# Kernel tuning notes

Measured on AMD Instinct MI355X. Metric: run time of the kernel, lower is better.

The kernel has to match this reference:

```python
import jax, jax.numpy as jnp
import numpy as np

K = 499  # kernel_size


def setup_inputs() -> dict:
    key = jax.random.key(0)
    k1, k2 = jax.random.split(key)
    B, F, T = 32, 64, 8000
    # nonnegative spectrogram input, shape (B, 1, F, T)
    x = jax.random.uniform(k1, (B, 1, F, T), dtype=jnp.float32)
    a = 0.90 + 0.099 * jax.random.uniform(k2, (F,), dtype=jnp.float32)
    w = jnp.ones((F,), dtype=jnp.float32)
    return {"x": x, "a": a, "w": w}


def _build_kernel(a, w, dtype):
    # powers[f, k] = a_f ** k, k = 0..K-2
    F = a.shape[0]
    powers = a[:, None] ** jnp.arange(K - 1, dtype=dtype)  # (F, K-1)
    C = 1.0 / powers.sum(axis=1)                            # (F,)
    neg = (-C * w)[:, None] * powers                        # (F, K-1)
    # pre-flip kernel = [1, neg_0, ..., neg_{K-2}]; flipped -> [neg_{K-2}, ..., neg_0, 1]
    kern = jnp.concatenate([neg[:, ::-1], jnp.ones((F, 1), dtype)], axis=1)  # (F, K)
    return kern[:, None, :]  # (F, 1, K) OIH, groups = F


def reference(x, a, w):
    dtype = x.dtype
    kern = _build_kernel(a.astype(dtype), w.astype(dtype), dtype)
    xs = x[:, 0]  # (B, F, T)
    # replicate (edge) pad on the left by K-1 along time
    xp = jnp.pad(xs, ((0, 0), (0, 0), (K - 1, 0)), mode="edge")
    y = jax.lax.conv_general_dilated(
        xp, kern,
        window_strides=(1,), padding="VALID",
        dimension_numbers=("NCH", "OIH", "NCH"),
        feature_group_count=xs.shape[1],
    )  # (B, F, T)
    return jnp.abs(y)[:, None]  # (B, 1, F, T)
```

## Files before the change

kernel.cpp:

```cpp
#include <hip/hip_runtime.h>
#include <math.h>


constexpr int T    = 8000;
constexpr int F    = 64;
constexpr int B    = 32;
constexpr int KM1  = 498;
constexpr int ROUND = 256;
constexpr int NROUND = (T + ROUND - 1) / ROUND;

__global__ __launch_bounds__(256) void willmore_scan_kernel(
    const float* __restrict__ x, const float* __restrict__ a,
    const float* __restrict__ w, float* __restrict__ out)
{
    const int wid  = (blockIdx.x * blockDim.x + threadIdx.x) >> 6;
    const int lane = threadIdx.x & 63;
    if (wid >= B * F) return;
    const int f = wid % F;

    const float* xr   = x   + (size_t)wid * T;
    float*       orow = out + (size_t)wid * T;

    const double ad = (double)a[f];
    double p = ad, a498d = 1.0;
    for (int e = KM1; e; e >>= 1) { if (e & 1) a498d *= p; p *= p; }
    const double sumgeo = (1.0 - a498d) / (1.0 - ad);
    const float  af     = (float)ad;
    const float  na498  = (float)(-a498d);
    const float  g      = (float)(1.0 / sumgeo) * w[f];
    const double a4d    = ad * ad * ad * ad;
    const float  alane  = (float)exp2(log2(a4d) * (double)lane);
    float wstep[6];
    double tpow = a4d;
    #pragma unroll
    for (int s = 0; s < 6; ++s) { wstep[s] = (float)tpow; tpow *= tpow; }
    const float a256 = (float)tpow;

    float S = xr[0] * (float)sumgeo;

    int tR = 0;
    for (int rnd = 0; rnd < NROUND; ++rnd, tR += ROUND) {
        const int tbase = tR + 4 * lane;
        const bool tail = (tR + ROUND > T);

        float4 xv;
        if (!tail) {
            xv = *(const float4*)(xr + tbase);
        } else {
            xv.x = xr[min(tbase,     T - 1)];
            xv.y = xr[min(tbase + 1, T - 1)];
            xv.z = xr[min(tbase + 2, T - 1)];
            xv.w = xr[min(tbase + 3, T - 1)];
        }

        const int lag = tbase - KM1;
        float l0, l1, l2, l3;
        if (lag >= 0 && !tail) {
            const float2* lp = (const float2*)(xr + lag);
            float2 la = lp[0], lb = lp[1];
            l0 = la.x; l1 = la.y; l2 = lb.x; l3 = lb.y;
        } else {
            l0 = xr[max(min(lag,     T - 1), 0)];
            l1 = xr[max(min(lag + 1, T - 1), 0)];
            l2 = xr[max(min(lag + 2, T - 1), 0)];
            l3 = xr[max(min(lag + 3, T - 1), 0)];
        }

        const float u0 = fmaf(na498, l0, xv.x);
        const float u1 = fmaf(na498, l1, xv.y);
        const float u2 = fmaf(na498, l2, xv.z);
        const float u3 = fmaf(na498, l3, xv.w);

        const float q0 = u0;
        const float q1 = fmaf(af, q0, u1);
        const float q2 = fmaf(af, q1, u2);
        const float q3 = fmaf(af, q2, u3);

        float G = q3;
        #pragma unroll
        for (int s = 0; s < 6; ++s) {
            const float gup = __shfl_up(G, 1 << s, 64);
            const float ws  = (lane >= (1 << s)) ? wstep[s] : 0.0f;
            G = fmaf(ws, gup, G);
        }
        float Gprev = __shfl_up(G, 1, 64);
        if (lane == 0) Gprev = 0.0f;

        float s0 = fmaf(alane, S, Gprev);
        const float y0 = fabsf(fmaf(-g, s0, xv.x));
        const float s1 = fmaf(af, s0, u0);
        const float y1 = fabsf(fmaf(-g, s1, xv.y));
        const float s2 = fmaf(af, s1, u1);
        const float y2 = fabsf(fmaf(-g, s2, xv.z));
        const float s3 = fmaf(af, s2, u2);
        const float y3 = fabsf(fmaf(-g, s3, xv.w));

        const float Slast = __shfl(G, 63, 64);
        S = fmaf(a256, S, Slast);

        if (!tail || (tbase + 3 < T)) {
            *(float4*)(orow + tbase) = make_float4(y0, y1, y2, y3);
        }
    }
}

extern "C" void kernel_launch(void* const* d_in, const int* in_sizes, int n_in,
                              void* d_out, int out_size, void* d_ws, size_t ws_size,
                              hipStream_t stream) {
    const float* x = (const float*)d_in[0];
    const float* a = (const float*)d_in[1];
    const float* w = (const float*)d_in[2];
    float* out = (float*)d_out;

    const int rows = B * F;
    const int threads = 256;
    const int blocks = rows * 64 / threads;
    hipLaunchKernelGGL(willmore_scan_kernel, dim3(blocks), dim3(threads), 0, stream,
                       x, a, w, out);
}
```

Before: 132.8 us.

## Split each row's scan into four time segments with windowed state initialization

Each row is now handled by one 256-thread block whose four wavefronts each scan a quarter of the time axis, instead of one wavefront scanning the whole row. Because the filter has finite support of 498 taps, each segment rebuilds its starting state directly from the preceding 512 samples using a weighted wavefront reduction. This shortens the serial chain of rounds per wavefront by about four times and should expose more latency hiding. The cost is some extra loads and arithmetic for the warm-up window, and possible precision differences from computing the initial state in float.

```diff
diff --git a/kernel.cpp b/kernel.cpp
--- a/kernel.cpp
+++ b/kernel.cpp
@@ -2,24 +2,27 @@
 #include <math.h>
 
 
-constexpr int T    = 8000;
-constexpr int F    = 64;
-constexpr int B    = 32;
-constexpr int KM1  = 498;
+constexpr int T     = 8000;
+constexpr int F     = 64;
+constexpr int B     = 32;
+constexpr int KM1   = 498;
+constexpr int NSEG  = 4;
+constexpr int SEGLEN = T / NSEG;
 constexpr int ROUND = 256;
-constexpr int NROUND = (T + ROUND - 1) / ROUND;
+constexpr int NFULL = SEGLEN / ROUND;
+constexpr int TAILN = SEGLEN - NFULL * ROUND;
 
 __global__ __launch_bounds__(256) void willmore_scan_kernel(
     const float* __restrict__ x, const float* __restrict__ a,
     const float* __restrict__ w, float* __restrict__ out)
 {
-    const int wid  = (blockIdx.x * blockDim.x + threadIdx.x) >> 6;
+    const int row  = blockIdx.x;
+    const int seg  = threadIdx.x >> 6;
     const int lane = threadIdx.x & 63;
-    if (wid >= B * F) return;
-    const int f = wid % F;
+    const int f = row % F;
 
-    const float* xr   = x   + (size_t)wid * T;
-    float*       orow = out + (size_t)wid * T;
+    const float* xr   = x   + (size_t)row * T;
+    float*       orow = out + (size_t)row * T;
 
     const double ad = (double)a[f];
     double p = ad, a498d = 1.0;
@@ -36,12 +39,40 @@
     for (int s = 0; s < 6; ++s) { wstep[s] = (float)tpow; tpow *= tpow; }
     const float a256 = (float)tpow;
 
-    float S = xr[0] * (float)sumgeo;
+    const int t0 = seg * SEGLEN;
 
-    int tR = 0;
-    for (int rnd = 0; rnd < NROUND; ++rnd, tR += ROUND) {
+    float S;
+    {
+        const int base = t0 - 512 + 8 * lane;
+        float xs[8];
+        if (t0 == 0) {
+            #pragma unroll
+            for (int i = 0; i < 8; ++i) xs[i] = xr[max(base + i, 0)];
+        } else {
+            const float4 v0 = *(const float4*)(xr + base);
+            const float4 v1 = *(const float4*)(xr + base + 4);
+            xs[0]=v0.x; xs[1]=v0.y; xs[2]=v0.z; xs[3]=v0.w;
+            xs[4]=v1.x; xs[5]=v1.y; xs[6]=v1.z; xs[7]=v1.w;
+        }
+        #pragma unroll
+        for (int i = 0; i < 8; ++i) { if (511 - 8*lane - i >= KM1) xs[i] = 0.0f; }
+        float h = xs[0];
+        #pragma unroll
+        for (int i = 1; i < 8; ++i) h = fmaf(h, af, xs[i]);
+        const int e = 504 - 8 * lane;
+        float wl = 1.0f, pb = af;
+        #pragma unroll
+        for (int s = 0; s < 9; ++s) { if (e & (1 << s)) wl *= pb; pb *= pb; }
+        float contrib = wl * h;
+        #pragma unroll
+        for (int s = 1; s < 64; s <<= 1) contrib += __shfl_xor(contrib, s, 64);
+        S = contrib;
+    }
+
+    int tR = t0;
+    for (int rnd = 0; rnd <= NFULL; ++rnd, tR += ROUND) {
+        const bool tail = (rnd == NFULL);
         const int tbase = tR + 4 * lane;
-        const bool tail = (tR + ROUND > T);
 
         float4 xv;
         if (!tail) {
@@ -57,7 +88,7 @@
         float l0, l1, l2, l3;
         if (lag >= 0 && !tail) {
             const float2* lp = (const float2*)(xr + lag);
-            float2 la = lp[0], lb = lp[1];
+            const float2 la = lp[0], lb = lp[1];
             l0 = la.x; l1 = la.y; l2 = lb.x; l3 = lb.y;
         } else {
             l0 = xr[max(min(lag,     T - 1), 0)];
@@ -71,8 +102,7 @@
         const float u2 = fmaf(na498, l2, xv.z);
         const float u3 = fmaf(na498, l3, xv.w);
 
-        const float q0 = u0;
-        const float q1 = fmaf(af, q0, u1);
+        const float q1 = fmaf(af, u0, u1);
         const float q2 = fmaf(af, q1, u2);
         const float q3 = fmaf(af, q2, u3);
 
@@ -86,7 +116,7 @@
         float Gprev = __shfl_up(G, 1, 64);
         if (lane == 0) Gprev = 0.0f;
 
-        float s0 = fmaf(alane, S, Gprev);
+        const float s0 = fmaf(alane, S, Gprev);
         const float y0 = fabsf(fmaf(-g, s0, xv.x));
         const float s1 = fmaf(af, s0, u0);
         const float y1 = fabsf(fmaf(-g, s1, xv.y));
@@ -95,10 +125,11 @@
         const float s3 = fmaf(af, s2, u2);
         const float y3 = fabsf(fmaf(-g, s3, xv.w));
 
-        const float Slast = __shfl(G, 63, 64);
-        S = fmaf(a256, S, Slast);
-
-        if (!tail || (tbase + 3 < T)) {
+        if (!tail) {
+            *(float4*)(orow + tbase) = make_float4(y0, y1, y2, y3);
+            const float Slast = __shfl(G, 63, 64);
+            S = fmaf(a256, S, Slast);
+        } else if (4 * lane < TAILN) {
             *(float4*)(orow + tbase) = make_float4(y0, y1, y2, y3);
         }
     }
@@ -112,9 +143,7 @@
     const float* w = (const float*)d_in[2];
     float* out = (float*)d_out;
 
-    const int rows = B * F;
-    const int threads = 256;
-    const int blocks = rows * 64 / threads;
-    hipLaunchKernelGGL(willmore_scan_kernel, dim3(blocks), dim3(threads), 0, stream,
+    const int blocks = B * F;
+    hipLaunchKernelGGL(willmore_scan_kernel, dim3(blocks), dim3(256), 0, stream,
                        x, a, w, out);
 }
```

Measured after the change: 122.5 us. 1.08x faster.
